# Kernel tuning notes

Measured on AMD Instinct MI355X. Metric: run time of the kernel, lower is better.

Reference implementation:

```python
import jax, jax.numpy as jnp
import numpy as np

N_QUBITS = 12
ENTANGLER_REPS = 2  # qml.layer(BasicEntanglerLayers, reps=2): 2 rings of CNOTs


def _apply_rx(state, theta, q, n):
    # state: (B, 2^n) complex; theta: (B,) per-sample RX angle on wire q
    B = state.shape[0]
    st = state.reshape(B, 2 ** q, 2, -1)
    c = jnp.cos(theta * 0.5)[:, None, None]
    s = jnp.sin(theta * 0.5)[:, None, None]
    s0, s1 = st[:, :, 0, :], st[:, :, 1, :]
    new0 = c * s0 - 1j * s * s1
    new1 = -1j * s * s0 + c * s1
    return jnp.stack([new0, new1], axis=2).reshape(B, -1)


def _apply_cnot(state, c, t, n):
    # CNOT with control wire c, target wire t (wire 0 = most significant bit)
    B = state.shape[0]
    st = state.reshape((B,) + (2,) * n)
    a0 = jnp.take(st, jnp.array([0]), axis=c + 1)
    a1 = jnp.take(st, jnp.array([1]), axis=c + 1)
    a1 = jnp.flip(a1, axis=t + 1)  # flip target when control = 1
    return jnp.concatenate([a0, a1], axis=c + 1).reshape(B, -1)


def quantum_latent(z, q_params):
    # Batched statevector simulation of: RX(z_i + p_i) on each wire,
    # then ENTANGLER_REPS rings of CNOT(i, (i+1)%n), measure <Z_i> per wire.
    B, n = z.shape
    theta = z + q_params[None, :]
    state = jnp.zeros((B, 2 ** n), dtype=jnp.complex64).at[:, 0].set(1.0)
    for q in range(n):
        state = _apply_rx(state, theta[:, q], q, n)
    for _ in range(ENTANGLER_REPS):
        for q in range(n):
            state = _apply_cnot(state, q, (q + 1) % n, n)
    probs = jnp.real(state * jnp.conj(state))  # (B, 2^n)
    expz = []
    for q in range(n):
        p = probs.reshape(B, 2 ** q, 2, -1)
        expz.append(p[:, :, 0, :].sum(axis=(1, 2)) - p[:, :, 1, :].sum(axis=(1, 2)))
    return jnp.stack(expz, axis=1)  # (B, n) float32


def setup_inputs() -> dict:
    key = jax.random.key(0)
    ks = jax.random.split(key, 16)
    B, D, H1, H2, L = 2048, 4096, 2048, 1024, N_QUBITS

    def lin(k, i, o):
        return (jax.random.normal(k, (o, i), jnp.float32) / np.sqrt(i)).astype(jnp.float32)

    return {
        "x": jax.random.normal(ks[0], (B, D), jnp.float32),
        "enc_w1": lin(ks[1], D, H1), "enc_b1": jnp.zeros((H1,), jnp.float32),
        "enc_w2": lin(ks[2], H1, H2), "enc_b2": jnp.zeros((H2,), jnp.float32),
        "enc_w3": lin(ks[3], H2, L), "enc_b3": jnp.zeros((L,), jnp.float32),
        "q_params": 0.1 * jax.random.normal(ks[4], (L,), jnp.float32),
        "dec_w1": lin(ks[5], L, H2), "dec_b1": jnp.zeros((H2,), jnp.float32),
        "dec_w2": lin(ks[6], H2, H1), "dec_b2": jnp.zeros((H1,), jnp.float32),
        "dec_w3": lin(ks[7], H1, D), "dec_b3": jnp.zeros((D,), jnp.float32),
    }


def reference(x, enc_w1, enc_b1, enc_w2, enc_b2, enc_w3, enc_b3, q_params,
              dec_w1, dec_b1, dec_w2, dec_b2, dec_w3, dec_b3):
    # encoder: Linear+ReLU (dropout=0 -> identity), Linear+ReLU, Linear
    h = jax.nn.relu(x @ enc_w1.T + enc_b1)
    h = jax.nn.relu(h @ enc_w2.T + enc_b2)
    z = h @ enc_w3.T + enc_b3  # (B, latent_dim)
    qz = quantum_latent(z, q_params)  # (B, latent_dim)
    # decoder (reversed hidden dims)
    h = jax.nn.relu(qz @ dec_w1.T + dec_b1)
    h = jax.nn.relu(h @ dec_w2.T + dec_b2)
    recon = h @ dec_w3.T + dec_b3  # (B, input_dim)
    return recon
```

## Files before the change

### kernel.cpp

```cpp
#include <hip/hip_runtime.h>
#include <hip/hip_bf16.h>


typedef __bf16 bf16x8 __attribute__((ext_vector_type(8)));
typedef __bf16 bf16x4 __attribute__((ext_vector_type(4)));
typedef float  f32x4  __attribute__((ext_vector_type(4)));

__device__ __forceinline__ void async16(const void* g, void* l) {
    __builtin_amdgcn_global_load_lds(
        (const __attribute__((address_space(1))) unsigned int*)g,
        (__attribute__((address_space(3))) unsigned int*)l,
        16, 0, 0);
}

template<int VM> __device__ __forceinline__ void wait_vm_lgkm0() {
    if constexpr (VM == 0)      asm volatile("s_waitcnt vmcnt(0) lgkmcnt(0)" ::: "memory");
    else if constexpr (VM == 4) asm volatile("s_waitcnt vmcnt(4) lgkmcnt(0)" ::: "memory");
    else if constexpr (VM == 6) asm volatile("s_waitcnt vmcnt(6) lgkmcnt(0)" ::: "memory");
    else if constexpr (VM == 8) asm volatile("s_waitcnt vmcnt(8) lgkmcnt(0)" ::: "memory");
    else static_assert(VM == 0 || VM == 4 || VM == 6 || VM == 8, "unsupported VM");
}

template <int BM, int BN, typename TOUT, bool RELU>
__global__ __launch_bounds__(256) void gemm_pipe(
    const __bf16* __restrict__ A, const __bf16* __restrict__ W,
    const float* __restrict__ bias, TOUT* __restrict__ C,
    int M, int N, int K)
{
    constexpr int CHA = BM / 32, CHB = BN / 32, LLOADS = CHA + CHB;
    constexpr int ABYTES = BM * 128, BUFB = (BM + BN) * 128;
    constexpr int WMR = BM / 2, WNC = BN / 2;
    constexpr int NI = WMR / 16, NJ = WNC / 16;

    extern __shared__ char smem[];

    const int t    = threadIdx.x;
    const int lane = t & 63;
    const int w    = t >> 6;
    const int bm   = blockIdx.y * BM;
    const int bn   = blockIdx.x * BN;

    const int sr  = lane >> 3;
    const int scs = (lane & 7) ^ sr;
    const __bf16* gA = A + (size_t)(bm + w * 8 + sr) * K + scs * 8;
    const __bf16* gB = W + (size_t)(bn + w * 8 + sr) * K + scs * 8;

    const int lm = lane & 15;
    const int lh = lane >> 4;
    const int wm = w >> 1, wn = w & 1;
    const int axor = lm & 7;

    f32x4 acc[NI][NJ] = {};

    auto STAGE = [&](int buf, int tt) {
        char* la = smem + buf * BUFB + w * 1024;
        char* lb = smem + buf * BUFB + ABYTES + w * 1024;
        const __bf16* ga = gA + (size_t)tt * 64;
        const __bf16* gb = gB + (size_t)tt * 64;
        #pragma unroll
        for (int j = 0; j < CHA; ++j) async16(ga + (size_t)32 * K * j, la + j * 4096);
        #pragma unroll
        for (int j = 0; j < CHB; ++j) async16(gb + (size_t)32 * K * j, lb + j * 4096);
    };

    auto COMPUTE = [&](int buf) {
        char* base = smem + buf * BUFB;
        bf16x8 a[2][NI], b[2][NJ];
        #pragma unroll
        for (int kh = 0; kh < 2; ++kh) {
            #pragma unroll
            for (int i = 0; i < NI; ++i)
                a[kh][i] = *(const bf16x8*)(base + (wm * WMR + i * 16 + lm) * 128
                                            + ((kh * 4 + lh) ^ axor) * 16);
            #pragma unroll
            for (int j = 0; j < NJ; ++j)
                b[kh][j] = *(const bf16x8*)(base + ABYTES + (wn * WNC + j * 16 + lm) * 128
                                            + ((kh * 4 + lh) ^ axor) * 16);
        }
        __builtin_amdgcn_s_setprio(1);
        #pragma unroll
        for (int kh = 0; kh < 2; ++kh)
            #pragma unroll
            for (int i = 0; i < NI; ++i)
                #pragma unroll
                for (int j = 0; j < NJ; ++j)
                    acc[i][j] = __builtin_amdgcn_mfma_f32_16x16x32_bf16(
                        a[kh][i], b[kh][j], acc[i][j], 0, 0, 0);
        __builtin_amdgcn_s_setprio(0);
    };

    const int NT = K >> 6;
    STAGE(0, 0);
    STAGE(1, 1);

    for (int tt = 0; tt < NT; ++tt) {
        if (tt < NT - 1) wait_vm_lgkm0<LLOADS>();
        else             wait_vm_lgkm0<0>();
        __builtin_amdgcn_s_barrier();
        __builtin_amdgcn_sched_barrier(0);
        COMPUTE(tt & 1);
        if (tt + 2 < NT) {
            asm volatile("s_waitcnt lgkmcnt(0)" ::: "memory");
            __builtin_amdgcn_s_barrier();
            __builtin_amdgcn_sched_barrier(0);
            STAGE(tt & 1, tt + 2);
        }
    }

    #pragma unroll
    for (int i = 0; i < NI; ++i) {
        const int row0 = bm + wm * WMR + i * 16 + lh * 4;
        #pragma unroll
        for (int j = 0; j < NJ; ++j) {
            const int col = bn + wn * WNC + j * 16 + lm;
            const float bv = bias[col];
            #pragma unroll
            for (int r = 0; r < 4; ++r) {
                float v = acc[i][j][r] + bv;
                if (RELU) v = fmaxf(v, 0.f);
                C[(size_t)(row0 + r) * N + col] = (TOUT)v;
            }
        }
    }
}

__device__ __forceinline__ void cvt8(const float* __restrict__ src,
                                     __bf16* __restrict__ dst, int g) {
    const float4* p = reinterpret_cast<const float4*>(src) + (size_t)g * 2;
    float4 a = p[0], b = p[1];
    bf16x8 v;
    v[0] = (__bf16)a.x; v[1] = (__bf16)a.y; v[2] = (__bf16)a.z; v[3] = (__bf16)a.w;
    v[4] = (__bf16)b.x; v[5] = (__bf16)b.y; v[6] = (__bf16)b.z; v[7] = (__bf16)b.w;
    reinterpret_cast<bf16x8*>(dst)[g] = v;
}

__global__ __launch_bounds__(256) void cvt_pair(
    const float* __restrict__ s0, __bf16* __restrict__ d0, int n0,
    const float* __restrict__ s1, __bf16* __restrict__ d1)
{
    int i = blockIdx.x * 256 + threadIdx.x;
    if (i < n0) cvt8(s0, d0, i);
    else        cvt8(s1, d1, i - n0);
}

__global__ __launch_bounds__(256) void cvt_triple(
    const float* __restrict__ s0, __bf16* __restrict__ d0, int n0,
    const float* __restrict__ s1, __bf16* __restrict__ d1, int n1,
    const float* __restrict__ s2, __bf16* __restrict__ d2)
{
    int i = blockIdx.x * 256 + threadIdx.x;
    if (i < n0)           cvt8(s0, d0, i);
    else if (i < n0 + n1) cvt8(s1, d1, i - n0);
    else                  cvt8(s2, d2, i - n0 - n1);
}

__constant__ unsigned short kSMask[12] = {
    0xAAB, 0xFFD, 0xFFA, 0xFF5, 0xFEA, 0xFD5,
    0xFAA, 0xF55, 0xEAA, 0xD55, 0xAAA, 0x555
};

__global__ __launch_bounds__(256) void enc3q_dec1(
    const float* __restrict__ H2,
    const float* __restrict__ W3,
    const float* __restrict__ b3,
    const float* __restrict__ qp,
    const float* __restrict__ dW1,
    const float* __restrict__ db1,
    __bf16* __restrict__ H3)
{
    const int b    = blockIdx.x;
    const int t    = threadIdx.x;
    const int lane = t & 63;
    const int wid  = t >> 6;

    float h[4];
    #pragma unroll
    for (int i = 0; i < 4; ++i) h[i] = H2[(size_t)b * 1024 + t + i * 256];

    __shared__ float wred[4][12];
    __shared__ float ctheta[12];
    __shared__ float qz[12];

    #pragma unroll 1
    for (int n = 0; n < 12; ++n) {
        float p = 0.f;
        #pragma unroll
        for (int i = 0; i < 4; ++i)
            p = fmaf(h[i], W3[n * 1024 + t + i * 256], p);
        #pragma unroll
        for (int off = 32; off > 0; off >>= 1)
            p += __shfl_down(p, off);
        if (lane == 0) wred[wid][n] = p;
    }
    __syncthreads();

    if (t < 12) {
        float z = wred[0][t] + wred[1][t] + wred[2][t] + wred[3][t]
                + b3[t] + qp[t];
        ctheta[t] = cosf(z);
    }
    __syncthreads();

    if (t < 12) {
        const unsigned m = kSMask[t];
        float prod = 1.f;
        #pragma unroll
        for (int j = 0; j < 12; ++j)
            if ((m >> j) & 1) prod *= ctheta[j];
        qz[t] = prod;
    }
    __syncthreads();

    bf16x4 v;
    #pragma unroll
    for (int j = 0; j < 4; ++j) {
        const int n = t * 4 + j;
        float acc = db1[n];
        #pragma unroll
        for (int k = 0; k < 12; ++k)
            acc = fmaf(qz[k], dW1[n * 12 + k], acc);
        v[j] = (__bf16)fmaxf(acc, 0.f);
    }
    *reinterpret_cast<bf16x4*>(&H3[(size_t)b * 1024 + t * 4]) = v;
}

extern "C" void kernel_launch(void* const* d_in, const int* in_sizes, int n_in,
                              void* d_out, int out_size, void* d_ws, size_t ws_size,
                              hipStream_t stream) {
    const float* x   = (const float*)d_in[0];
    const float* w1  = (const float*)d_in[1];
    const float* b1  = (const float*)d_in[2];
    const float* w2  = (const float*)d_in[3];
    const float* b2  = (const float*)d_in[4];
    const float* w3  = (const float*)d_in[5];
    const float* b3  = (const float*)d_in[6];
    const float* qp  = (const float*)d_in[7];
    const float* dw1 = (const float*)d_in[8];
    const float* db1 = (const float*)d_in[9];
    const float* dw2 = (const float*)d_in[10];
    const float* db2 = (const float*)d_in[11];
    const float* dw3 = (const float*)d_in[12];
    const float* db3 = (const float*)d_in[13];
    float* out = (float*)d_out;

    const int B = 2048, D = 4096, H1 = 2048, H2 = 1024;

    char* ws = (char*)d_ws;
    __bf16* xb   = (__bf16*)(ws);
    __bf16* dw3b = (__bf16*)(ws);
    __bf16* w1b  = (__bf16*)(ws + 16777216);
    float*  h2f  = (float*) (ws + 16777216);
    __bf16* w2b  = (__bf16*)(ws + 25165824);
    __bf16* h3b  = (__bf16*)(ws + 25165824);
    __bf16* dw2b = (__bf16*)(ws + 29360128);
    __bf16* h1b  = (__bf16*)(ws + 33554432);
    __bf16* h4b  = (__bf16*)(ws + 33554432);

    dim3 blk(256);

    cvt_pair<<<dim3(8192), blk, 0, stream>>>(x, xb, 1048576, w1, w1b);

    gemm_pipe<128, 64, __bf16, true><<<dim3(H1 / 64, B / 128), blk, 49152, stream>>>(
        xb, w1b, b1, h1b, B, H1, D);

    cvt_triple<<<dim3(6144), blk, 0, stream>>>(w2, w2b, 262144,
                                               dw2, dw2b, 262144,
                                               dw3, dw3b);

    gemm_pipe<64, 64, float, true><<<dim3(H2 / 64, B / 64), blk, 32768, stream>>>(
        h1b, w2b, b2, h2f, B, H2, H1);

    enc3q_dec1<<<dim3(B), blk, 0, stream>>>(h2f, w3, b3, qp, dw1, db1, h3b);

    gemm_pipe<128, 64, __bf16, true><<<dim3(H1 / 64, B / 128), blk, 49152, stream>>>(
        h3b, dw2b, db2, h4b, B, H1, H2);

    gemm_pipe<128, 128, float, false><<<dim3(D / 128, B / 128), blk, 65536, stream>>>(
        h4b, dw3b, db3, out, B, D, H1);
}
```

Before: 153.8 us.

## Swizzle GEMM block order across XCDs and shrink final GEMM tile

Launches each GEMM on a 1D grid and remaps block indices so consecutive blocks land on the same XCD (round-robin by 8) with column-major tile order, improving L2 reuse of shared A/W tiles. The inner compute loop now loads LDS fragments per k-half right before its MFMAs, cutting register pressure. The last GEMM moves from a 128x128 tile to 128x64, doubling the block count to 1024 for better CU fill at the cost of more redundant A loads.

```diff
diff --git a/kernel.cpp b/kernel.cpp
--- a/kernel.cpp
+++ b/kernel.cpp
@@ -13,7 +13,7 @@
         16, 0, 0);
 }
 
-template<int VM> __device__ __forceinline__ void wait_vm_lgkm0() {
+template<int VM> __device__ __forceinline__ void wait_vm() {
     if constexpr (VM == 0)      asm volatile("s_waitcnt vmcnt(0) lgkmcnt(0)" ::: "memory");
     else if constexpr (VM == 4) asm volatile("s_waitcnt vmcnt(4) lgkmcnt(0)" ::: "memory");
     else if constexpr (VM == 6) asm volatile("s_waitcnt vmcnt(6) lgkmcnt(0)" ::: "memory");
@@ -21,32 +21,43 @@
     else static_assert(VM == 0 || VM == 4 || VM == 6 || VM == 8, "unsupported VM");
 }
 
-template <int BM, int BN, typename TOUT, bool RELU>
+__device__ __forceinline__ void cvt8(const float* __restrict__ src,
+                                     __bf16* __restrict__ dst, int g) {
+    const float4* p = reinterpret_cast<const float4*>(src) + (size_t)g * 2;
+    float4 a = p[0], b = p[1];
+    bf16x8 v;
+    v[0] = (__bf16)a.x; v[1] = (__bf16)a.y; v[2] = (__bf16)a.z; v[3] = (__bf16)a.w;
+    v[4] = (__bf16)b.x; v[5] = (__bf16)b.y; v[6] = (__bf16)b.z; v[7] = (__bf16)b.w;
+    reinterpret_cast<bf16x8*>(dst)[g] = v;
+}
+
+template <int BM, int BN, int GX, int GY, typename TOUT, bool RELU>
 __global__ __launch_bounds__(256) void gemm_pipe(
     const __bf16* __restrict__ A, const __bf16* __restrict__ W,
     const float* __restrict__ bias, TOUT* __restrict__ C,
     int M, int N, int K)
 {
-    constexpr int CHA = BM / 32, CHB = BN / 32, LLOADS = CHA + CHB;
+    constexpr int CHA = BM / 32, CHB = BN / 32, L = CHA + CHB;
     constexpr int ABYTES = BM * 128, BUFB = (BM + BN) * 128;
     constexpr int WMR = BM / 2, WNC = BN / 2;
     constexpr int NI = WMR / 16, NJ = WNC / 16;
 
     extern __shared__ char smem[];
 
-    const int t    = threadIdx.x;
-    const int lane = t & 63;
-    const int w    = t >> 6;
-    const int bm   = blockIdx.y * BM;
-    const int bn   = blockIdx.x * BN;
+    const int t = threadIdx.x, lane = t & 63, w = t >> 6;
+
+    constexpr int CPX = (GX * GY) >> 3;
+    const int lin = blockIdx.x;
+    const int swz = (lin & 7) * CPX + (lin >> 3);
+    const int bm = (swz % GY) * BM;
+    const int bn = (swz / GY) * BN;
 
     const int sr  = lane >> 3;
     const int scs = (lane & 7) ^ sr;
     const __bf16* gA = A + (size_t)(bm + w * 8 + sr) * K + scs * 8;
     const __bf16* gB = W + (size_t)(bn + w * 8 + sr) * K + scs * 8;
 
-    const int lm = lane & 15;
-    const int lh = lane >> 4;
+    const int lm = lane & 15, lh = lane >> 4;
     const int wm = w >> 1, wn = w & 1;
     const int axor = lm & 7;
 
@@ -64,29 +75,26 @@
     };
 
     auto COMPUTE = [&](int buf) {
-        char* base = smem + buf * BUFB;
-        bf16x8 a[2][NI], b[2][NJ];
+        const char* base = smem + buf * BUFB;
         #pragma unroll
         for (int kh = 0; kh < 2; ++kh) {
+            const int sl = ((kh * 4 + lh) ^ axor) * 16;
+            bf16x8 a[NI], b[NJ];
             #pragma unroll
             for (int i = 0; i < NI; ++i)
-                a[kh][i] = *(const bf16x8*)(base + (wm * WMR + i * 16 + lm) * 128
-                                            + ((kh * 4 + lh) ^ axor) * 16);
+                a[i] = *(const bf16x8*)(base + (wm * WMR + i * 16 + lm) * 128 + sl);
             #pragma unroll
             for (int j = 0; j < NJ; ++j)
-                b[kh][j] = *(const bf16x8*)(base + ABYTES + (wn * WNC + j * 16 + lm) * 128
-                                            + ((kh * 4 + lh) ^ axor) * 16);
-        }
-        __builtin_amdgcn_s_setprio(1);
-        #pragma unroll
-        for (int kh = 0; kh < 2; ++kh)
+                b[j] = *(const bf16x8*)(base + ABYTES + (wn * WNC + j * 16 + lm) * 128 + sl);
+            __builtin_amdgcn_s_setprio(1);
             #pragma unroll
             for (int i = 0; i < NI; ++i)
                 #pragma unroll
                 for (int j = 0; j < NJ; ++j)
                     acc[i][j] = __builtin_amdgcn_mfma_f32_16x16x32_bf16(
-                        a[kh][i], b[kh][j], acc[i][j], 0, 0, 0);
-        __builtin_amdgcn_s_setprio(0);
+                        a[i], b[j], acc[i][j], 0, 0, 0);
+            __builtin_amdgcn_s_setprio(0);
+        }
     };
 
     const int NT = K >> 6;
@@ -94,8 +102,8 @@
     STAGE(1, 1);
 
     for (int tt = 0; tt < NT; ++tt) {
-        if (tt < NT - 1) wait_vm_lgkm0<LLOADS>();
-        else             wait_vm_lgkm0<0>();
+        if (tt < NT - 1) wait_vm<L>();
+        else             wait_vm<0>();
         __builtin_amdgcn_s_barrier();
         __builtin_amdgcn_sched_barrier(0);
         COMPUTE(tt & 1);
@@ -122,16 +130,6 @@
             }
         }
     }
-}
-
-__device__ __forceinline__ void cvt8(const float* __restrict__ src,
-                                     __bf16* __restrict__ dst, int g) {
-    const float4* p = reinterpret_cast<const float4*>(src) + (size_t)g * 2;
-    float4 a = p[0], b = p[1];
-    bf16x8 v;
-    v[0] = (__bf16)a.x; v[1] = (__bf16)a.y; v[2] = (__bf16)a.z; v[3] = (__bf16)a.w;
-    v[4] = (__bf16)b.x; v[5] = (__bf16)b.y; v[6] = (__bf16)b.z; v[7] = (__bf16)b.w;
-    reinterpret_cast<bf16x8*>(dst)[g] = v;
 }
 
 __global__ __launch_bounds__(256) void cvt_pair(
@@ -245,6 +243,17 @@
 
     const int B = 2048, D = 4096, H1 = 2048, H2 = 1024;
 
+    static int attr_done = 0;
+    if (!attr_done) {
+        hipFuncSetAttribute((const void*)&gemm_pipe<128, 64, 32, 16, __bf16, true>,
+                            hipFuncAttributeMaxDynamicSharedMemorySize, 49152);
+        hipFuncSetAttribute((const void*)&gemm_pipe<64, 64, 16, 32, float, true>,
+                            hipFuncAttributeMaxDynamicSharedMemorySize, 32768);
+        hipFuncSetAttribute((const void*)&gemm_pipe<128, 64, 64, 16, float, false>,
+                            hipFuncAttributeMaxDynamicSharedMemorySize, 49152);
+        attr_done = 1;
+    }
+
     char* ws = (char*)d_ws;
     __bf16* xb   = (__bf16*)(ws);
     __bf16* dw3b = (__bf16*)(ws);
@@ -260,21 +269,21 @@
 
     cvt_pair<<<dim3(8192), blk, 0, stream>>>(x, xb, 1048576, w1, w1b);
 
-    gemm_pipe<128, 64, __bf16, true><<<dim3(H1 / 64, B / 128), blk, 49152, stream>>>(
+    gemm_pipe<128, 64, 32, 16, __bf16, true><<<dim3(512), blk, 49152, stream>>>(
         xb, w1b, b1, h1b, B, H1, D);
 
     cvt_triple<<<dim3(6144), blk, 0, stream>>>(w2, w2b, 262144,
                                                dw2, dw2b, 262144,
                                                dw3, dw3b);
 
-    gemm_pipe<64, 64, float, true><<<dim3(H2 / 64, B / 64), blk, 32768, stream>>>(
+    gemm_pipe<64, 64, 16, 32, float, true><<<dim3(512), blk, 32768, stream>>>(
         h1b, w2b, b2, h2f, B, H2, H1);
 
     enc3q_dec1<<<dim3(B), blk, 0, stream>>>(h2f, w3, b3, qp, dw1, db1, h3b);
 
-    gemm_pipe<128, 64, __bf16, true><<<dim3(H1 / 64, B / 128), blk, 49152, stream>>>(
+    gemm_pipe<128, 64, 32, 16, __bf16, true><<<dim3(512), blk, 49152, stream>>>(
         h3b, dw2b, db2, h4b, B, H1, H2);
 
-    gemm_pipe<128, 128, float, false><<<dim3(D / 128, B / 128), blk, 65536, stream>>>(
+    gemm_pipe<128, 64, 64, 16, float, false><<<dim3(1024), blk, 49152, stream>>>(
         h4b, dw3b, db3, out, B, D, H1);
 }
```

After: 166.8 us. 8.5% more time.
